# Optimization experiments

Hardware: AMD Instinct MI355X
Metric: run time of the kernel (lower is better)

The kernel has to match this reference:

```python
import jax, jax.numpy as jnp
import numpy as np

BETA = 1e-07


def setup_inputs() -> dict:
    key = jax.random.key(0)
    k1, k2 = jax.random.split(key)
    predict = jax.random.normal(k1, (8192, 4096), dtype=jnp.float32)
    target = jax.random.normal(k2, (8192, 4096), dtype=jnp.float32)
    return {"predict": predict, "target": target}


def reference(predict, target):
    # Per-row negative Pearson correlation, vectorized over the batch dim.
    xc = predict - predict.mean(axis=1, keepdims=True)  # [B, T]
    yc = target - target.mean(axis=1, keepdims=True)    # [B, T]
    num = (xc * yc).sum(axis=1)                          # [B]
    den = jnp.sqrt((xc * xc).sum(axis=1) + BETA) * jnp.sqrt((yc * yc).sum(axis=1) + BETA)
    p = 1.0 - num / den                                  # [B]
    return p.mean()
```

## Files before the change

### kernel.cpp

```cpp
#include <hip/hip_runtime.h>

#define ROW_LEN 4096
#define N_ROWS  8192
#define BETA    1e-7f

__global__ __launch_bounds__(256) void row_pearson_kernel(
    const float* __restrict__ x, const float* __restrict__ y,
    float* __restrict__ p_row) {
    const int row = blockIdx.x;
    const int tid = threadIdx.x;

    const float4* __restrict__ xr =
        reinterpret_cast<const float4*>(x + (size_t)row * ROW_LEN);
    const float4* __restrict__ yr =
        reinterpret_cast<const float4*>(y + (size_t)row * ROW_LEN);

    float sx = 0.f, sy = 0.f, sxy = 0.f, sxx = 0.f, syy = 0.f;

#pragma unroll
    for (int i = 0; i < 4; ++i) {
        float4 a = xr[tid + i * 256];
        float4 b = yr[tid + i * 256];
        sx  += a.x + a.y + a.z + a.w;
        sy  += b.x + b.y + b.z + b.w;
        sxy += a.x * b.x + a.y * b.y + a.z * b.z + a.w * b.w;
        sxx += a.x * a.x + a.y * a.y + a.z * a.z + a.w * a.w;
        syy += b.x * b.x + b.y * b.y + b.z * b.z + b.w * b.w;
    }

#pragma unroll
    for (int off = 32; off > 0; off >>= 1) {
        sx  += __shfl_down(sx, off);
        sy  += __shfl_down(sy, off);
        sxy += __shfl_down(sxy, off);
        sxx += __shfl_down(sxx, off);
        syy += __shfl_down(syy, off);
    }

    __shared__ float red[4][5];
    const int wave = tid >> 6;
    const int lane = tid & 63;
    if (lane == 0) {
        red[wave][0] = sx;
        red[wave][1] = sy;
        red[wave][2] = sxy;
        red[wave][3] = sxx;
        red[wave][4] = syy;
    }
    __syncthreads();

    if (tid == 0) {
        float Sx = 0.f, Sy = 0.f, Sxy = 0.f, Sxx = 0.f, Syy = 0.f;
#pragma unroll
        for (int w = 0; w < 4; ++w) {
            Sx  += red[w][0];
            Sy  += red[w][1];
            Sxy += red[w][2];
            Sxx += red[w][3];
            Syy += red[w][4];
        }
        const float invT = 1.0f / (float)ROW_LEN;
        float num = Sxy - Sx * Sy * invT;
        float xx  = Sxx - Sx * Sx * invT;
        float yy  = Syy - Sy * Sy * invT;
        float den = sqrtf(xx + BETA) * sqrtf(yy + BETA);
        p_row[row] = 1.0f - num / den;
    }
}

__global__ __launch_bounds__(256) void mean_kernel(
    const float* __restrict__ p_row, float* __restrict__ out) {
    const int tid = threadIdx.x;
    float s = 0.f;
#pragma unroll
    for (int i = 0; i < N_ROWS / 256; ++i) {
        s += p_row[tid + i * 256];
    }
#pragma unroll
    for (int off = 32; off > 0; off >>= 1) {
        s += __shfl_down(s, off);
    }
    __shared__ float red[4];
    const int wave = tid >> 6;
    const int lane = tid & 63;
    if (lane == 0) red[wave] = s;
    __syncthreads();
    if (tid == 0) {
        float tot = red[0] + red[1] + red[2] + red[3];
        out[0] = tot * (1.0f / (float)N_ROWS);
    }
}

extern "C" void kernel_launch(void* const* d_in, const int* in_sizes, int n_in,
                              void* d_out, int out_size, void* d_ws, size_t ws_size,
                              hipStream_t stream) {
    const float* predict = (const float*)d_in[0];
    const float* target  = (const float*)d_in[1];
    float* out   = (float*)d_out;
    float* p_row = (float*)d_ws;

    row_pearson_kernel<<<N_ROWS, 256, 0, stream>>>(predict, target, p_row);
    mean_kernel<<<1, 256, 0, stream>>>(p_row, out);
}
```

Measured before the change: 45.34 us.

## Assign one row per wave and fuse final mean via last-block atomic counter

Each wave now reduces a full row independently, with four rows per block, which removes the cross-wave shared-memory reduction for row statistics. The separate mean kernel is removed. Instead, each block increments a global counter and the last block sums the per-row results. A memset resets the counter every call, which adds an extra operation, and the atomic ordering adds a small serialization tail.

```diff
diff --git a/kernel.cpp b/kernel.cpp
--- a/kernel.cpp
+++ b/kernel.cpp
@@ -3,26 +3,31 @@
 #define ROW_LEN 4096
 #define N_ROWS  8192
 #define BETA    1e-7f
+#define NBLOCKS 2048
+#define RPB     4
 
-__global__ __launch_bounds__(256) void row_pearson_kernel(
+__global__ __launch_bounds__(256) void pearson_fused_kernel(
     const float* __restrict__ x, const float* __restrict__ y,
-    float* __restrict__ p_row) {
-    const int row = blockIdx.x;
-    const int tid = threadIdx.x;
+    float* __restrict__ p_row, unsigned int* __restrict__ counter,
+    float* __restrict__ out) {
+    const int tid  = threadIdx.x;
+    const int wave = tid >> 6;
+    const int lane = tid & 63;
+    const int row  = blockIdx.x * RPB + wave;
 
     const float4* __restrict__ xr =
-        reinterpret_cast<const float4*>(x + (size_t)row * ROW_LEN);
+        reinterpret_cast<const float4*>(x) + (size_t)row * (ROW_LEN / 4);
     const float4* __restrict__ yr =
-        reinterpret_cast<const float4*>(y + (size_t)row * ROW_LEN);
+        reinterpret_cast<const float4*>(y) + (size_t)row * (ROW_LEN / 4);
 
     float sx = 0.f, sy = 0.f, sxy = 0.f, sxx = 0.f, syy = 0.f;
 
-#pragma unroll
-    for (int i = 0; i < 4; ++i) {
-        float4 a = xr[tid + i * 256];
-        float4 b = yr[tid + i * 256];
-        sx  += a.x + a.y + a.z + a.w;
-        sy  += b.x + b.y + b.z + b.w;
+#pragma unroll 8
+    for (int k = 0; k < 16; ++k) {
+        float4 a = xr[lane + 64 * k];
+        float4 b = yr[lane + 64 * k];
+        sx  += (a.x + a.y) + (a.z + a.w);
+        sy  += (b.x + b.y) + (b.z + b.w);
         sxy += a.x * b.x + a.y * b.y + a.z * b.z + a.w * b.w;
         sxx += a.x * a.x + a.y * a.y + a.z * a.z + a.w * a.w;
         syy += b.x * b.x + b.y * b.y + b.z * b.z + b.w * b.w;
@@ -37,57 +42,42 @@
         syy += __shfl_down(syy, off);
     }
 
-    __shared__ float red[4][5];
-    const int wave = tid >> 6;
-    const int lane = tid & 63;
     if (lane == 0) {
-        red[wave][0] = sx;
-        red[wave][1] = sy;
-        red[wave][2] = sxy;
-        red[wave][3] = sxx;
-        red[wave][4] = syy;
+        const float invT = 1.0f / (float)ROW_LEN;
+        float num = sxy - sx * sy * invT;
+        float xx  = sxx - sx * sx * invT;
+        float yy  = syy - sy * sy * invT;
+        float p   = 1.0f - num / (sqrtf(xx + BETA) * sqrtf(yy + BETA));
+        __hip_atomic_store(&p_row[row], p, __ATOMIC_RELAXED,
+                           __HIP_MEMORY_SCOPE_AGENT);
+    }
+
+    __syncthreads();
+
+    __shared__ int lastFlag;
+    if (tid == 0) {
+        unsigned int prev = __hip_atomic_fetch_add(
+            counter, 1u, __ATOMIC_ACQ_REL, __HIP_MEMORY_SCOPE_AGENT);
+        lastFlag = (prev == NBLOCKS - 1) ? 1 : 0;
     }
     __syncthreads();
+    if (!lastFlag) return;
 
-    if (tid == 0) {
-        float Sx = 0.f, Sy = 0.f, Sxy = 0.f, Sxx = 0.f, Syy = 0.f;
-#pragma unroll
-        for (int w = 0; w < 4; ++w) {
-            Sx  += red[w][0];
-            Sy  += red[w][1];
-            Sxy += red[w][2];
-            Sxx += red[w][3];
-            Syy += red[w][4];
-        }
-        const float invT = 1.0f / (float)ROW_LEN;
-        float num = Sxy - Sx * Sy * invT;
-        float xx  = Sxx - Sx * Sx * invT;
-        float yy  = Syy - Sy * Sy * invT;
-        float den = sqrtf(xx + BETA) * sqrtf(yy + BETA);
-        p_row[row] = 1.0f - num / den;
-    }
-}
-
-__global__ __launch_bounds__(256) void mean_kernel(
-    const float* __restrict__ p_row, float* __restrict__ out) {
-    const int tid = threadIdx.x;
     float s = 0.f;
 #pragma unroll
     for (int i = 0; i < N_ROWS / 256; ++i) {
-        s += p_row[tid + i * 256];
+        s += __hip_atomic_load(&p_row[tid + i * 256], __ATOMIC_RELAXED,
+                               __HIP_MEMORY_SCOPE_AGENT);
     }
 #pragma unroll
     for (int off = 32; off > 0; off >>= 1) {
         s += __shfl_down(s, off);
     }
     __shared__ float red[4];
-    const int wave = tid >> 6;
-    const int lane = tid & 63;
     if (lane == 0) red[wave] = s;
     __syncthreads();
     if (tid == 0) {
-        float tot = red[0] + red[1] + red[2] + red[3];
-        out[0] = tot * (1.0f / (float)N_ROWS);
+        out[0] = (red[0] + red[1] + red[2] + red[3]) * (1.0f / (float)N_ROWS);
     }
 }
 
@@ -96,9 +86,14 @@
                               hipStream_t stream) {
     const float* predict = (const float*)d_in[0];
     const float* target  = (const float*)d_in[1];
-    float* out   = (float*)d_out;
+    float* out = (float*)d_out;
+
     float* p_row = (float*)d_ws;
+    unsigned int* counter =
+        (unsigned int*)((char*)d_ws + N_ROWS * sizeof(float));
 
-    row_pearson_kernel<<<N_ROWS, 256, 0, stream>>>(predict, target, p_row);
-    mean_kernel<<<1, 256, 0, stream>>>(p_row, out);
+    hipMemsetAsync(counter, 0, sizeof(unsigned int), stream);
+
+    pearson_fused_kernel<<<NBLOCKS, 256, 0, stream>>>(predict, target, p_row,
+                                                      counter, out);
 }
```

New measurement: 109.7 us. 142% more time.
